# Kernel tuning notes

Hardware: AMD Instinct MI355X
Metric: run time of the kernel (lower is better)

The kernel has to match this reference:

```python
import jax, jax.numpy as jnp
import numpy as np

N_NODES = 50000
N_EDGES = 800000
D_IN = 128
D_SH = 16
D_OUT = 128
N_PATHS = 64


def setup_inputs() -> dict:
    key = jax.random.key(0)
    k1, k2, k3, k4, k5, k6, k7, k8 = jax.random.split(key, 8)
    x = jax.random.normal(k1, (N_NODES, D_IN), dtype=jnp.float32)
    sh = jax.random.normal(k2, (N_EDGES, D_SH), dtype=jnp.float32)
    coeff = jax.random.normal(k3, (N_PATHS,), dtype=jnp.float32)
    src = jax.random.randint(k4, (N_EDGES,), 0, N_NODES, dtype=jnp.int64)
    dst = jax.random.randint(k5, (N_EDGES,), 0, N_NODES, dtype=jnp.int64)
    ki = jax.random.randint(k6, (N_PATHS,), 0, D_IN, dtype=jnp.int32)
    kj = jax.random.randint(k7, (N_PATHS,), 0, D_SH, dtype=jnp.int32)
    ko = jax.random.randint(k8, (N_PATHS,), 0, D_OUT, dtype=jnp.int32)
    return {"x": x, "sh": sh, "coeff": coeff, "src": src, "dst": dst,
            "ki": ki, "kj": kj, "ko": ko}


def reference(x, sh, coeff, src, dst, ki, kj, ko):
    # 1) gather: index_select node features by edge source -> [E, D_in]
    xg = x[src]
    # 2) segmented tensor product: sum over sparse paths p of
    #    coeff[p] * xg[:, ki[p]] * sh[:, kj[p]] accumulated into output slot ko[p]
    vals = coeff[None, :] * xg[:, ki] * sh[:, kj]          # [E, P]
    msg = jnp.zeros((sh.shape[0], D_OUT), dtype=x.dtype).at[:, ko].add(vals)  # [E, D_out]
    # 3) scatter_add messages into per-node output -> [N, D_out]
    out = jnp.zeros((x.shape[0], D_OUT), dtype=x.dtype).at[dst].add(msg)
    return out
```

## Files before the change

### kernel.cpp

```cpp
#include <hip/hip_runtime.h>
#include <hip/hip_fp16.h>

#define N_NODES 50000
#define N_EDGES 800000
#define D_IN    128
#define D_SH    16
#define D_OUT   128
#define N_PATHS 64

#define SEGN    128
#define NSEG    391
#define NSEGP   512
#define CAPE    2560
#define EPB     6250
#define BINB    128
#define XCB     3125
#define BLK     256

#define QN      32
#define QCAP    1024
#define NQB     (NSEG * 4)

#define OFF_META 2048
#define OFF_SH16 (OFF_META + NSEG*CAPE*4)
#define OFF_XCH  (OFF_SH16 + NSEG*CAPE*32)

__global__ __launch_bounds__(BLK) void bin_kernel(
        const float* __restrict__ x, const int* __restrict__ ki,
        const float* __restrict__ sh, const int* __restrict__ src,
        const int* __restrict__ dst, int* __restrict__ segcnt,
        int* __restrict__ meta, __half* __restrict__ sh16,
        __half* __restrict__ xc_h) {
    __shared__ int lcnt[NSEGP];
    __shared__ int lstart[NSEGP];
    __shared__ int lofs[NSEGP];
    __shared__ int gbase[NSEGP];
    __shared__ unsigned short sorted_[EPB];
    __shared__ unsigned short dstsh[EPB];
    const int tid = threadIdx.x;

    if (blockIdx.x < BINB) {
        const int e0 = blockIdx.x * EPB;
        for (int s = tid; s < NSEGP; s += BLK) lcnt[s] = 0;
        __syncthreads();
        for (int i = tid; i < EPB; i += BLK) {
            int d = dst[e0 + i];
            dstsh[i] = (unsigned short)d;
            atomicAdd(&lcnt[d >> 7], 1);
        }
        __syncthreads();
        if (tid < 64) {
            int b8 = tid * 8, v[8], s0 = 0;
            #pragma unroll
            for (int k = 0; k < 8; ++k) { v[k] = lcnt[b8 + k]; s0 += v[k]; }
            int run = s0;
            #pragma unroll
            for (int off = 1; off < 64; off <<= 1) {
                int y = __shfl_up(run, off);
                if (tid >= off) run += y;
            }
            int acc = run - s0;
            #pragma unroll
            for (int k = 0; k < 8; ++k) {
                lstart[b8 + k] = acc; lofs[b8 + k] = acc; acc += v[k];
            }
        } else {
            for (int s = tid - 64; s < NSEG; s += BLK - 64) {
                int c = lcnt[s];
                gbase[s] = c ? atomicAdd(&segcnt[s], c) : 0;
            }
        }
        __syncthreads();
        for (int i = tid; i < EPB; i += BLK) {
            int r = atomicAdd(&lofs[dstsh[i] >> 7], 1);
            sorted_[r] = (unsigned short)i;
        }
        __syncthreads();
        for (int j = tid; j < EPB; j += BLK) {
            int i = sorted_[j];
            int e = e0 + i;
            int d = dstsh[i];
            int s = d >> 7;
            int pos = gbase[s] + (j - lstart[s]);
            if (pos < CAPE) {
                size_t gi = (size_t)s * CAPE + pos;
                meta[gi] = src[e] | ((d & 127) << 16);
                const float4* shv = (const float4*)(sh + (size_t)e * D_SH);
                float4 f0 = shv[0], f1 = shv[1], f2 = shv[2], f3 = shv[3];
                union { __half2 h[8]; int4 v[2]; } u;
                u.h[0] = __floats2half2_rn(f0.x, f0.y);
                u.h[1] = __floats2half2_rn(f0.z, f0.w);
                u.h[2] = __floats2half2_rn(f1.x, f1.y);
                u.h[3] = __floats2half2_rn(f1.z, f1.w);
                u.h[4] = __floats2half2_rn(f2.x, f2.y);
                u.h[5] = __floats2half2_rn(f2.z, f2.w);
                u.h[6] = __floats2half2_rn(f3.x, f3.y);
                u.h[7] = __floats2half2_rn(f3.z, f3.w);
                int4* dp = (int4*)(sh16 + gi * 16);
                dp[0] = u.v[0]; dp[1] = u.v[1];
            }
        }
    } else {
        const int b2   = blockIdx.x - BINB;
        const int lane = tid & 63;
        const int w    = tid >> 6;
        const int nb   = b2 * 16 + w * 4;
        const int kil  = ki[lane];
        float x0 = x[(size_t)(nb + 0) * D_IN + kil];
        float x1 = x[(size_t)(nb + 1) * D_IN + kil];
        float x2 = x[(size_t)(nb + 2) * D_IN + kil];
        float x3 = x[(size_t)(nb + 3) * D_IN + kil];
        xc_h[(size_t)(nb + 0) * N_PATHS + lane] = __float2half_rn(x0);
        xc_h[(size_t)(nb + 1) * N_PATHS + lane] = __float2half_rn(x1);
        xc_h[(size_t)(nb + 2) * N_PATHS + lane] = __float2half_rn(x2);
        xc_h[(size_t)(nb + 3) * N_PATHS + lane] = __float2half_rn(x3);
    }
}

__global__ __launch_bounds__(BLK) void node_kernel(
        const int* __restrict__ segcnt, const int* __restrict__ meta,
        const __half* __restrict__ sh16, const __half* __restrict__ xc_h,
        const float* __restrict__ coeff, const int* __restrict__ kj,
        const int* __restrict__ ko, float* __restrict__ out) {
    __shared__ int cnt_l[QN];
    __shared__ int nstart[QN + 1];
    __shared__ int ncur[QN];
    __shared__ unsigned short csr_src[QCAP];
    __shared__ unsigned short csr_idx[QCAP];
    __shared__ float srow[BLK / 64][D_OUT];
    const int tid  = threadIdx.x;
    const int lane = tid & 63;
    const int w    = tid >> 6;
    const int seg  = blockIdx.x >> 2;
    const int q    = blockIdx.x & 3;
    const int nb_l = q * QN;
    const int n_e  = min(segcnt[seg], CAPE);
    const size_t mb = (size_t)seg * CAPE;
    const __half* shb = sh16 + mb * 16;

    if (tid < QN) cnt_l[tid] = 0;
    __syncthreads();
    for (int i = tid; i < n_e; i += BLK) {
        unsigned int u = (unsigned)(((meta[mb + i] >> 16) & 127) - nb_l);
        if (u < QN) atomicAdd(&cnt_l[u], 1);
    }
    __syncthreads();
    if (tid < QN) {
        int v = cnt_l[tid];
        int run = v;
        #pragma unroll
        for (int off = 1; off < QN; off <<= 1) {
            int y = __shfl_up(run, off);
            if (tid >= off) run += y;
        }
        nstart[tid] = run - v;
        ncur[tid]   = run - v;
        if (tid == QN - 1) nstart[QN] = run;
    }
    __syncthreads();
    for (int i = tid; i < n_e; i += BLK) {
        int m = meta[mb + i];
        unsigned int u = (unsigned)(((m >> 16) & 127) - nb_l);
        if (u < QN) {
            int r = atomicAdd(&ncur[u], 1);
            if (r < QCAP) {
                csr_src[r] = (unsigned short)(m & 0xFFFF);
                csr_idx[r] = (unsigned short)i;
            }
        }
    }
    __syncthreads();

    const int   kj_p = kj[lane];
    const int   ko_p = ko[lane];
    const float c_p  = coeff[lane];

    #pragma unroll 1
    for (int k = 0; k < QN / (BLK / 64); ++k) {
        const int c    = w * (QN / (BLK / 64)) + k;
        const int node = seg * SEGN + nb_l + c;
        const int st   = min(nstart[c], QCAP);
        const int en   = min(nstart[c + 1], QCAP);
        float acc = 0.0f;
        int j = st;
        for (; j + 16 <= en; j += 16) {
            float xv[16], sv[16];
            #pragma unroll
            for (int u8 = 0; u8 < 16; ++u8) {
                int s = csr_src[j + u8];
                int i = csr_idx[j + u8];
                xv[u8] = __half2float(xc_h[(size_t)s * N_PATHS + lane]);
                sv[u8] = __half2float(shb[(size_t)i * 16 + kj_p]);
            }
            #pragma unroll
            for (int u8 = 0; u8 < 16; ++u8) acc += xv[u8] * sv[u8];
        }
        if (j < en) {
            float xv[16], sv[16];
            #pragma unroll
            for (int u8 = 0; u8 < 16; ++u8) {
                int jj = j + u8;
                int jc = jj < en ? jj : st;
                int s = csr_src[jc];
                int i = csr_idx[jc];
                xv[u8] = __half2float(xc_h[(size_t)s * N_PATHS + lane]);
                sv[u8] = __half2float(shb[(size_t)i * 16 + kj_p]);
            }
            #pragma unroll
            for (int u8 = 0; u8 < 16; ++u8)
                if (j + u8 < en) acc += xv[u8] * sv[u8];
        }
        acc *= c_p;
        if (node < N_NODES) {
            srow[w][lane]      = 0.0f;
            srow[w][lane + 64] = 0.0f;
            atomicAdd(&srow[w][ko_p], acc);
            float r0 = srow[w][lane];
            float r1 = srow[w][lane + 64];
            float* orow = out + (size_t)node * D_OUT;
            orow[lane]      = r0;
            orow[lane + 64] = r1;
        }
    }
}

extern "C" void kernel_launch(void* const* d_in, const int* in_sizes, int n_in,
                              void* d_out, int out_size, void* d_ws, size_t ws_size,
                              hipStream_t stream) {
    const float* x     = (const float*)d_in[0];
    const float* sh    = (const float*)d_in[1];
    const float* coeff = (const float*)d_in[2];
    const int*   src   = (const int*)d_in[3];
    const int*   dst   = (const int*)d_in[4];
    const int*   ki    = (const int*)d_in[5];
    const int*   kj    = (const int*)d_in[6];
    const int*   ko    = (const int*)d_in[7];
    float* out = (float*)d_out;

    char* p = (char*)d_ws;
    int*    segcnt = (int*)p;
    int*    meta   = (int*)(p + OFF_META);
    __half* sh16   = (__half*)(p + OFF_SH16);
    __half* xc_h   = (__half*)(p + OFF_XCH);
    (void)ws_size;

    hipMemsetAsync(p, 0, 2048, stream);
    bin_kernel<<<BINB + XCB, BLK, 0, stream>>>(
        x, ki, sh, src, dst, segcnt, meta, sh16, xc_h);
    node_kernel<<<NQB, BLK, 0, stream>>>(
        segcnt, meta, sh16, xc_h, coeff, kj, ko, out);
}
```

Measured before the change: 233.3 us.

## Split binning into separate scatter and gather kernels with smaller edge chunks

Splits the fused bin kernel into two launches: one that gathers the selected x columns into a half-precision compact array, and one that bins edges by destination segment. The binning now uses 400 blocks of 512 threads, each handling 2000 edges instead of 6250, so more of the GPU is busy during the sort and scatter phase. src is staged into shared memory during the counting pass, so it is no longer re-read at random from global memory. This adds an extra kernel launch and serialises the two formerly concurrent phases. Smaller chunks also mean more global atomics on segcnt and less locality in each block's sorted writes.

```diff
diff --git a/kernel.cpp b/kernel.cpp
--- a/kernel.cpp
+++ b/kernel.cpp
@@ -12,9 +12,11 @@
 #define NSEG    391
 #define NSEGP   512
 #define CAPE    2560
-#define EPB     6250
-#define BINB    128
-#define XCB     3125
+
+#define EPB     2000
+#define BINB    400
+#define BLKA    512
+#define XCB     1563
 #define BLK     256
 
 #define QN      32
@@ -25,95 +27,96 @@
 #define OFF_SH16 (OFF_META + NSEG*CAPE*4)
 #define OFF_XCH  (OFF_SH16 + NSEG*CAPE*32)
 
-__global__ __launch_bounds__(BLK) void bin_kernel(
-        const float* __restrict__ x, const int* __restrict__ ki,
+__global__ __launch_bounds__(BLKA) void bin_scatter(
         const float* __restrict__ sh, const int* __restrict__ src,
         const int* __restrict__ dst, int* __restrict__ segcnt,
-        int* __restrict__ meta, __half* __restrict__ sh16,
-        __half* __restrict__ xc_h) {
+        int* __restrict__ meta, __half* __restrict__ sh16) {
     __shared__ int lcnt[NSEGP];
     __shared__ int lstart[NSEGP];
     __shared__ int lofs[NSEGP];
     __shared__ int gbase[NSEGP];
     __shared__ unsigned short sorted_[EPB];
     __shared__ unsigned short dstsh[EPB];
+    __shared__ unsigned short srcsh[EPB];
     const int tid = threadIdx.x;
-
-    if (blockIdx.x < BINB) {
-        const int e0 = blockIdx.x * EPB;
-        for (int s = tid; s < NSEGP; s += BLK) lcnt[s] = 0;
-        __syncthreads();
-        for (int i = tid; i < EPB; i += BLK) {
-            int d = dst[e0 + i];
-            dstsh[i] = (unsigned short)d;
-            atomicAdd(&lcnt[d >> 7], 1);
-        }
-        __syncthreads();
-        if (tid < 64) {
-            int b8 = tid * 8, v[8], s0 = 0;
-            #pragma unroll
-            for (int k = 0; k < 8; ++k) { v[k] = lcnt[b8 + k]; s0 += v[k]; }
-            int run = s0;
-            #pragma unroll
-            for (int off = 1; off < 64; off <<= 1) {
-                int y = __shfl_up(run, off);
-                if (tid >= off) run += y;
-            }
-            int acc = run - s0;
-            #pragma unroll
-            for (int k = 0; k < 8; ++k) {
-                lstart[b8 + k] = acc; lofs[b8 + k] = acc; acc += v[k];
-            }
-        } else {
-            for (int s = tid - 64; s < NSEG; s += BLK - 64) {
-                int c = lcnt[s];
-                gbase[s] = c ? atomicAdd(&segcnt[s], c) : 0;
-            }
-        }
-        __syncthreads();
-        for (int i = tid; i < EPB; i += BLK) {
-            int r = atomicAdd(&lofs[dstsh[i] >> 7], 1);
-            sorted_[r] = (unsigned short)i;
-        }
-        __syncthreads();
-        for (int j = tid; j < EPB; j += BLK) {
-            int i = sorted_[j];
-            int e = e0 + i;
-            int d = dstsh[i];
-            int s = d >> 7;
-            int pos = gbase[s] + (j - lstart[s]);
-            if (pos < CAPE) {
-                size_t gi = (size_t)s * CAPE + pos;
-                meta[gi] = src[e] | ((d & 127) << 16);
-                const float4* shv = (const float4*)(sh + (size_t)e * D_SH);
-                float4 f0 = shv[0], f1 = shv[1], f2 = shv[2], f3 = shv[3];
-                union { __half2 h[8]; int4 v[2]; } u;
-                u.h[0] = __floats2half2_rn(f0.x, f0.y);
-                u.h[1] = __floats2half2_rn(f0.z, f0.w);
-                u.h[2] = __floats2half2_rn(f1.x, f1.y);
-                u.h[3] = __floats2half2_rn(f1.z, f1.w);
-                u.h[4] = __floats2half2_rn(f2.x, f2.y);
-                u.h[5] = __floats2half2_rn(f2.z, f2.w);
-                u.h[6] = __floats2half2_rn(f3.x, f3.y);
-                u.h[7] = __floats2half2_rn(f3.z, f3.w);
-                int4* dp = (int4*)(sh16 + gi * 16);
-                dp[0] = u.v[0]; dp[1] = u.v[1];
-            }
+    const int e0  = blockIdx.x * EPB;
+
+    lcnt[tid] = 0;
+    __syncthreads();
+    for (int i = tid; i < EPB; i += BLKA) {
+        int d = dst[e0 + i];
+        int s = src[e0 + i];
+        dstsh[i] = (unsigned short)d;
+        srcsh[i] = (unsigned short)s;
+        atomicAdd(&lcnt[d >> 7], 1);
+    }
+    __syncthreads();
+    if (tid < 64) {
+        int b8 = tid * 8, v[8], s0 = 0;
+        #pragma unroll
+        for (int k = 0; k < 8; ++k) { v[k] = lcnt[b8 + k]; s0 += v[k]; }
+        int run = s0;
+        #pragma unroll
+        for (int off = 1; off < 64; off <<= 1) {
+            int y = __shfl_up(run, off);
+            if (tid >= off) run += y;
+        }
+        int acc = run - s0;
+        #pragma unroll
+        for (int k = 0; k < 8; ++k) {
+            lstart[b8 + k] = acc; lofs[b8 + k] = acc; acc += v[k];
         }
     } else {
-        const int b2   = blockIdx.x - BINB;
-        const int lane = tid & 63;
-        const int w    = tid >> 6;
-        const int nb   = b2 * 16 + w * 4;
-        const int kil  = ki[lane];
-        float x0 = x[(size_t)(nb + 0) * D_IN + kil];
-        float x1 = x[(size_t)(nb + 1) * D_IN + kil];
-        float x2 = x[(size_t)(nb + 2) * D_IN + kil];
-        float x3 = x[(size_t)(nb + 3) * D_IN + kil];
-        xc_h[(size_t)(nb + 0) * N_PATHS + lane] = __float2half_rn(x0);
-        xc_h[(size_t)(nb + 1) * N_PATHS + lane] = __float2half_rn(x1);
-        xc_h[(size_t)(nb + 2) * N_PATHS + lane] = __float2half_rn(x2);
-        xc_h[(size_t)(nb + 3) * N_PATHS + lane] = __float2half_rn(x3);
+        for (int s = tid - 64; s < NSEG; s += BLKA - 64) {
+            int c = lcnt[s];
+            gbase[s] = c ? atomicAdd(&segcnt[s], c) : 0;
+        }
+    }
+    __syncthreads();
+    for (int i = tid; i < EPB; i += BLKA) {
+        int r = atomicAdd(&lofs[dstsh[i] >> 7], 1);
+        sorted_[r] = (unsigned short)i;
+    }
+    __syncthreads();
+    for (int j = tid; j < EPB; j += BLKA) {
+        int i = sorted_[j];
+        int d = dstsh[i];
+        int s = d >> 7;
+        int pos = gbase[s] + (j - lstart[s]);
+        if (pos < CAPE) {
+            size_t gi = (size_t)s * CAPE + pos;
+            meta[gi] = (int)srcsh[i] | ((d & 127) << 16);
+            const float4* shv = (const float4*)(sh + (size_t)(e0 + i) * D_SH);
+            float4 f0 = shv[0], f1 = shv[1], f2 = shv[2], f3 = shv[3];
+            union { __half2 h[8]; int4 v[2]; } u;
+            u.h[0] = __floats2half2_rn(f0.x, f0.y);
+            u.h[1] = __floats2half2_rn(f0.z, f0.w);
+            u.h[2] = __floats2half2_rn(f1.x, f1.y);
+            u.h[3] = __floats2half2_rn(f1.z, f1.w);
+            u.h[4] = __floats2half2_rn(f2.x, f2.y);
+            u.h[5] = __floats2half2_rn(f2.z, f2.w);
+            u.h[6] = __floats2half2_rn(f3.x, f3.y);
+            u.h[7] = __floats2half2_rn(f3.z, f3.w);
+            int4* dp = (int4*)(sh16 + gi * 16);
+            dp[0] = u.v[0]; dp[1] = u.v[1];
+        }
+    }
+}
+
+__global__ __launch_bounds__(BLKA) void bin_xc(
+        const float* __restrict__ x, const int* __restrict__ ki,
+        __half* __restrict__ xc_h) {
+    const int tid  = threadIdx.x;
+    const int lane = tid & 63;
+    const int w    = tid >> 6;
+    const int nb   = blockIdx.x * 32 + w * 4;
+    const int kil  = ki[lane];
+    #pragma unroll
+    for (int k = 0; k < 4; ++k) {
+        int n = nb + k;
+        if (n < N_NODES)
+            xc_h[(size_t)n * N_PATHS + lane] =
+                __float2half_rn(x[(size_t)n * D_IN + kil]);
     }
 }
 
@@ -245,8 +248,9 @@
     (void)ws_size;
 
     hipMemsetAsync(p, 0, 2048, stream);
-    bin_kernel<<<BINB + XCB, BLK, 0, stream>>>(
-        x, ki, sh, src, dst, segcnt, meta, sh16, xc_h);
+    bin_xc<<<XCB, BLKA, 0, stream>>>(x, ki, xc_h);
+    bin_scatter<<<BINB, BLKA, 0, stream>>>(
+        sh, src, dst, segcnt, meta, sh16);
     node_kernel<<<NQB, BLK, 0, stream>>>(
         segcnt, meta, sh16, xc_h, coeff, kj, ko, out);
 }
```

Result: faster. 217.5 us (-6.8%).
